# Optimization experiments

Measured on AMD Instinct MI355X. Metric: run time of the kernel, lower is better.

Reference implementation:

```python
import jax, jax.numpy as jnp
import numpy as np

N_NODES = 50000
N_EDGES = 800000
N_GRAPHS = 512
IN_FEATS = 256
HIDDEN = 128
OUT_FEATS = 128


def _lin(key, fan_in, fan_out):
    return jax.random.normal(key, (fan_in, fan_out), jnp.float32) * (1.0 / np.sqrt(fan_in))


def setup_inputs() -> dict:
    key = jax.random.key(0)
    ks = jax.random.split(key, 16)
    x = jax.random.normal(ks[0], (N_NODES, IN_FEATS), jnp.float32)
    edge_index = jax.random.randint(ks[1], (2, N_EDGES), 0, N_NODES, jnp.int32)
    batch = jnp.sort(jax.random.randint(ks[2], (N_NODES,), 0, N_GRAPHS, jnp.int32))
    return {
        "x": x,
        "edge_index": edge_index,
        "batch": batch,
        "num_graphs": N_GRAPHS,
        # TD branch GCN params
        "td_W1": _lin(ks[3], IN_FEATS, HIDDEN), "td_b1": jnp.zeros((HIDDEN,), jnp.float32),
        "td_W2": _lin(ks[4], HIDDEN, OUT_FEATS), "td_b2": jnp.zeros((OUT_FEATS,), jnp.float32),
        # BU branch GCN params
        "bu_W1": _lin(ks[5], IN_FEATS, HIDDEN), "bu_b1": jnp.zeros((HIDDEN,), jnp.float32),
        "bu_W2": _lin(ks[6], HIDDEN, OUT_FEATS), "bu_b2": jnp.zeros((OUT_FEATS,), jnp.float32),
        # proj_head: Linear(256,256) -> ReLU -> Linear(256,128)
        "pw1": _lin(ks[7], OUT_FEATS * 2, 256), "pb1": jnp.zeros((256,), jnp.float32),
        "pw2": _lin(ks[8], 256, 128), "pb2": jnp.zeros((128,), jnp.float32),
    }


def gcn_conv(h_in, W, b, src, dst, n_nodes):
    """PyG GCNConv: self-loops + symmetric normalization D^-1/2 (A+I) D^-1/2 X W + b."""
    h = h_in @ W  # [N, out]
    ones = jnp.ones(src.shape[0], h.dtype)
    deg = jax.ops.segment_sum(ones, dst, num_segments=n_nodes) + 1.0  # +1 for self-loop
    dinv = jax.lax.rsqrt(deg)  # deg >= 1 always
    norm = dinv[src] * dinv[dst]  # [E]
    agg = jax.ops.segment_sum(h[src] * norm[:, None], dst, num_segments=n_nodes)
    agg = agg + h * (dinv * dinv)[:, None]  # self-loop edge contribution
    return agg + b


def reference(x, edge_index, batch, num_graphs,
              td_W1, td_b1, td_W2, td_b2,
              bu_W1, bu_b1, bu_W2, bu_b2,
              pw1, pb1, pw2, pb2):
    n = x.shape[0]
    src, dst = edge_index[0], edge_index[1]

    def branch(W1, b1, W2, b2, s, d):
        h = jax.nn.relu(gcn_conv(x, W1, b1, s, d, n))
        # dropout is identity in eval mode
        h = gcn_conv(h, W2, b2, s, d, n)
        return jax.ops.segment_sum(h, batch, num_segments=num_graphs)  # global_add_pool

    td = branch(td_W1, td_b1, td_W2, td_b2, src, dst)
    bu = branch(bu_W1, bu_b1, bu_W2, bu_b2, dst, src)  # flipped edge_index
    h = jnp.concatenate([bu, td], axis=1)  # [G, 2*out_feats]
    h = jax.nn.relu(h @ pw1 + pb1) @ pw2 + pb2
    return h
```

## Files before the change

kernel.cpp:

```cpp
#include <hip/hip_runtime.h>

#define N_NODES 50000
#define N_PAD   50048
#define N_EDGES 800000
#define N_GRAPHS 512
#define F_IN 256
#define F_H 128
#define F_CAT 256

#define BSHIFT 9
#define NB 98
#define CAP 10240
#define EPB 3125
#define GEMM_BLOCKS 782

typedef __attribute__((ext_vector_type(8))) short short8;
typedef __attribute__((ext_vector_type(4))) float f32x4;
typedef unsigned int uint;
typedef unsigned short ushort;

static __device__ __forceinline__ ushort f2bf(float f) {
    uint u = __float_as_uint(f);
    u += 0x7FFF + ((u >> 16) & 1);
    return (ushort)(u >> 16);
}
static __device__ __forceinline__ float bflo(uint v) { return __uint_as_float(v << 16); }
static __device__ __forceinline__ float bfhi(uint v) { return __uint_as_float(v & 0xFFFF0000u); }
static __device__ __forceinline__ float bfu(ushort v) { return __uint_as_float((uint)v << 16); }

#define GLL(g, l) __builtin_amdgcn_global_load_lds( \
    (const __attribute__((address_space(1))) unsigned int*)(g), \
    (__attribute__((address_space(3))) unsigned int*)(l), 16, 0, 0)

__global__ __launch_bounds__(256) void gemm_scatter_kernel(
        const float* __restrict__ x, const ushort* __restrict__ Bt,
        ushort* __restrict__ C,
        const int* __restrict__ ei, int* __restrict__ gcur,
        uint* __restrict__ ebuf_td, uint* __restrict__ ebuf_bu) {
    __shared__ __align__(16) ushort As[128 * 32];
    __shared__ __align__(16) ushort Bs[128 * 32];
    __shared__ int lcnt[256];
    __shared__ int lbase[256];
    int tid = threadIdx.x;

    if (blockIdx.x < GEMM_BLOCKS) {
        int wave = tid >> 6, lane = tid & 63, quad = lane >> 4, l16 = lane & 15;
        size_t bm = (size_t)(blockIdx.x >> 1) * 128;
        size_t bn = (size_t)(blockIdx.x & 1) * 128;

        f32x4 acc[2][8];
        const f32x4 z4 = {0.f, 0.f, 0.f, 0.f};
#pragma unroll
        for (int i = 0; i < 2; i++)
#pragma unroll
            for (int j = 0; j < 8; j++) acc[i][j] = z4;

        int ar = tid >> 3;
        int akq = (tid & 7) * 4;
        int cb0 = wave * 64;
        int cb1 = 256 + wave * 64;
        int c0 = cb0 + lane, c1 = cb1 + lane;
        int r0 = c0 >> 2, s0 = (c0 & 3) * 8;
        int r1 = c1 >> 2, s1 = (c1 & 3) * 8;
        const ushort* b0p = Bt + (bn + r0) * 256 + s0;
        const ushort* b1p = Bt + (bn + r1) * 256 + s1;
        ushort* lB0 = Bs + cb0 * 8;
        ushort* lB1 = Bs + cb1 * 8;

        for (int kb = 0; kb < 8; kb++) {
            int k0 = kb * 32;
            float4 av[4];
#pragma unroll
            for (int j = 0; j < 4; j++) {
                size_t grow = bm + ar + j * 32;
                if (grow < N_NODES)
                    av[j] = *(const float4*)(x + grow * F_IN + k0 + akq);
                else
                    av[j] = make_float4(0.f, 0.f, 0.f, 0.f);
            }
            __syncthreads();
            GLL(b0p + k0, lB0);
            GLL(b1p + k0, lB1);
#pragma unroll
            for (int j = 0; j < 4; j++) {
                ushort4 u;
                u.x = f2bf(av[j].x); u.y = f2bf(av[j].y);
                u.z = f2bf(av[j].z); u.w = f2bf(av[j].w);
                *(ushort4*)(As + (ar + j * 32) * 32 + akq) = u;
            }
            __syncthreads();
            short8 af0 = *(const short8*)(As + (wave * 32 + l16) * 32 + quad * 8);
            short8 af1 = *(const short8*)(As + (wave * 32 + 16 + l16) * 32 + quad * 8);
#pragma unroll
            for (int ct = 0; ct < 8; ct++) {
                short8 bfr = *(const short8*)(Bs + (ct * 16 + l16) * 32 + quad * 8);
                acc[0][ct] = __builtin_amdgcn_mfma_f32_16x16x32_bf16(af0, bfr, acc[0][ct], 0, 0, 0);
                acc[1][ct] = __builtin_amdgcn_mfma_f32_16x16x32_bf16(af1, bfr, acc[1][ct], 0, 0, 0);
            }
        }
#pragma unroll
        for (int rt = 0; rt < 2; rt++) {
#pragma unroll
            for (int r = 0; r < 4; r++) {
                size_t row = bm + wave * 32 + rt * 16 + quad * 4 + r;
#pragma unroll
                for (int ct = 0; ct < 8; ct++) {
                    C[row * 256 + bn + ct * 16 + l16] = f2bf(acc[rt][ct][r]);
                }
            }
        }
    } else {
        lcnt[tid] = 0;
        __syncthreads();
        int e0 = (blockIdx.x - GEMM_BLOCKS) * EPB;
        for (int k = tid; k < EPB; k += 256) {
            int i = e0 + k;
            int s = ei[i], d = ei[N_EDGES + i];
            atomicAdd(&lcnt[d >> BSHIFT], 1);
            atomicAdd(&lcnt[128 + (s >> BSHIFT)], 1);
        }
        __syncthreads();
        if (tid < 2 * NB) {
            int dir = tid / NB, b = tid % NB;
            int c = lcnt[dir * 128 + b];
            lbase[dir * 128 + b] = c ? atomicAdd(&gcur[dir * NB + b], c) : 0;
        }
        __syncthreads();
        lcnt[tid] = 0;
        __syncthreads();
        for (int k = tid; k < EPB; k += 256) {
            int i = e0 + k;
            int s = ei[i], d = ei[N_EDGES + i];
            int bd = d >> BSHIFT, bs = s >> BSHIFT;
            int p = atomicAdd(&lcnt[bd], 1) + lbase[bd];
            ebuf_td[(size_t)bd * CAP + p] = (uint)s | ((uint)(d & 511) << 16);
            int q = atomicAdd(&lcnt[128 + bs], 1) + lbase[128 + bs];
            ebuf_bu[(size_t)bs * CAP + q] = (uint)d | ((uint)(s & 511) << 16);
        }
    }
}

__global__ __launch_bounds__(256) void csr_build_kernel(
        const uint* __restrict__ ebuf_td, const uint* __restrict__ ebuf_bu,
        const int* __restrict__ gcur,
        int* off_td, int* off_bu, ushort* deg_td, ushort* deg_bu,
        float* dinv_td, float* dinv_bu, ushort* csr_td, ushort* csr_bu) {
    int b = blockIdx.x, dir = blockIdx.y;
    const uint* ebuf = dir ? ebuf_bu : ebuf_td;
    int* off     = dir ? off_bu : off_td;
    ushort* deg  = dir ? deg_bu : deg_td;
    float* dinv  = dir ? dinv_bu : dinv_td;
    ushort* csr  = dir ? csr_bu : csr_td;
    __shared__ int cntL[512], offL[512], sm[256];
    int tid = threadIdx.x;
    cntL[tid] = 0; cntL[tid + 256] = 0;
    __syncthreads();
    int rbeg = b * CAP;
    int rend = rbeg + gcur[dir * NB + b];
    for (int k = rbeg + tid; k < rend; k += 256)
        atomicAdd(&cntL[ebuf[k] >> 16], 1);
    __syncthreads();
    int a0 = cntL[tid * 2], a1 = cntL[tid * 2 + 1];
    int ps = a0 + a1;
    sm[tid] = ps;
    __syncthreads();
    for (int o = 1; o < 256; o <<= 1) {
        int u = (tid >= o) ? sm[tid - o] : 0;
        __syncthreads();
        sm[tid] += u;
        __syncthreads();
    }
    int excl = sm[tid] - ps;
    offL[tid * 2] = excl;
    offL[tid * 2 + 1] = excl + a0;
    __syncthreads();
    int nbase = b << BSHIFT;
#pragma unroll
    for (int j = 0; j < 2; j++) {
        int nloc = tid + j * 256;
        int n = nbase + nloc;
        if (n < N_NODES) {
            off[n] = rbeg + offL[nloc];
            int c = cntL[nloc];
            deg[n] = (ushort)c;
            dinv[n] = rsqrtf((float)c + 1.0f);
        }
    }
    if (b == NB - 1) {
        int n = N_NODES + tid;
        if (n < N_PAD) dinv[n] = 1.0f;
    }
    cntL[tid] = offL[tid];
    cntL[tid + 256] = offL[tid + 256];
    __syncthreads();
    for (int k = rbeg + tid; k < rend; k += 256) {
        uint e = ebuf[k];
        int slot = atomicAdd(&cntL[e >> 16], 1);
        csr[rbeg + slot] = (ushort)(e & 0xFFFF);
    }
}

__global__ __launch_bounds__(256) void scale_kernel(
        ushort* __restrict__ linb,
        const float* __restrict__ dinv_td, const float* __restrict__ dinv_bu) {
    size_t i = (size_t)blockIdx.x * 256 + threadIdx.x;
    int row = (int)(i >> 5);
    int c8 = ((int)i & 31) * 8;
    float dv = (c8 < F_H) ? dinv_td[row] : dinv_bu[row];
    uint4 v = ((uint4*)linb)[i];
    uint4 o;
    o.x = (uint)f2bf(bflo(v.x) * dv) | ((uint)f2bf(bfhi(v.x) * dv) << 16);
    o.y = (uint)f2bf(bflo(v.y) * dv) | ((uint)f2bf(bfhi(v.y) * dv) << 16);
    o.z = (uint)f2bf(bflo(v.z) * dv) | ((uint)f2bf(bfhi(v.z) * dv) << 16);
    o.w = (uint)f2bf(bflo(v.w) * dv) | ((uint)f2bf(bfhi(v.w) * dv) << 16);
    ((uint4*)linb)[i] = o;
}

__global__ void prep_w_kernel(const float* __restrict__ td_W1, const float* __restrict__ bu_W1,
                              const float* __restrict__ td_W2, const float* __restrict__ bu_W2,
                              ushort* __restrict__ Bt1, ushort* __restrict__ Wt2) {
    int n = blockIdx.x;
    int k = threadIdx.x;
    float w1 = (n < F_H) ? td_W1[(size_t)k * F_H + n] : bu_W1[(size_t)k * F_H + (n - F_H)];
    Bt1[(size_t)n * 256 + k] = f2bf(w1);
    if (k < 128) {
        float w2 = (n < F_H) ? bu_W2[(size_t)k * F_H + n]
                             : td_W2[(size_t)k * F_H + (n - F_H)];
        Wt2[(size_t)k * 256 + n] = f2bf(w2);
    }
}

static __device__ __forceinline__ void gather_node(
        const ushort* __restrict__ base, const ushort* __restrict__ csr,
        int kb, int ke, int half, float a[4]) {
    float p[4] = {0.f, 0.f, 0.f, 0.f};
    float q[4] = {0.f, 0.f, 0.f, 0.f};
    float r[4] = {0.f, 0.f, 0.f, 0.f};
    int k = kb;
    for (; k + 16 <= ke; k += 16) {
        int i0 = csr[k + half],      i1 = csr[k + 2 + half];
        int i2 = csr[k + 4 + half],  i3 = csr[k + 6 + half];
        int i4 = csr[k + 8 + half],  i5 = csr[k + 10 + half];
        int i6 = csr[k + 12 + half], i7 = csr[k + 14 + half];
        uint2 v0 = *(const uint2*)(base + (size_t)i0 * F_CAT);
        uint2 v1 = *(const uint2*)(base + (size_t)i1 * F_CAT);
        uint2 v2 = *(const uint2*)(base + (size_t)i2 * F_CAT);
        uint2 v3 = *(const uint2*)(base + (size_t)i3 * F_CAT);
        uint2 v4 = *(const uint2*)(base + (size_t)i4 * F_CAT);
        uint2 v5 = *(const uint2*)(base + (size_t)i5 * F_CAT);
        uint2 v6 = *(const uint2*)(base + (size_t)i6 * F_CAT);
        uint2 v7 = *(const uint2*)(base + (size_t)i7 * F_CAT);
        a[0] += bflo(v0.x); a[1] += bfhi(v0.x); a[2] += bflo(v0.y); a[3] += bfhi(v0.y);
        p[0] += bflo(v1.x); p[1] += bfhi(v1.x); p[2] += bflo(v1.y); p[3] += bfhi(v1.y);
        q[0] += bflo(v2.x); q[1] += bfhi(v2.x); q[2] += bflo(v2.y); q[3] += bfhi(v2.y);
        r[0] += bflo(v3.x); r[1] += bfhi(v3.x); r[2] += bflo(v3.y); r[3] += bfhi(v3.y);
        a[0] += bflo(v4.x); a[1] += bfhi(v4.x); a[2] += bflo(v4.y); a[3] += bfhi(v4.y);
        p[0] += bflo(v5.x); p[1] += bfhi(v5.x); p[2] += bflo(v5.y); p[3] += bfhi(v5.y);
        q[0] += bflo(v6.x); q[1] += bfhi(v6.x); q[2] += bflo(v6.y); q[3] += bfhi(v6.y);
        r[0] += bflo(v7.x); r[1] += bfhi(v7.x); r[2] += bflo(v7.y); r[3] += bfhi(v7.y);
    }
    for (; k + 8 <= ke; k += 8) {
        int i0 = csr[k + half],     i1 = csr[k + 2 + half];
        int i2 = csr[k + 4 + half], i3 = csr[k + 6 + half];
        uint2 v0 = *(const uint2*)(base + (size_t)i0 * F_CAT);
        uint2 v1 = *(const uint2*)(base + (size_t)i1 * F_CAT);
        uint2 v2 = *(const uint2*)(base + (size_t)i2 * F_CAT);
        uint2 v3 = *(const uint2*)(base + (size_t)i3 * F_CAT);
        a[0] += bflo(v0.x); a[1] += bfhi(v0.x); a[2] += bflo(v0.y); a[3] += bfhi(v0.y);
        p[0] += bflo(v1.x); p[1] += bfhi(v1.x); p[2] += bflo(v1.y); p[3] += bfhi(v1.y);
        q[0] += bflo(v2.x); q[1] += bfhi(v2.x); q[2] += bflo(v2.y); q[3] += bfhi(v2.y);
        r[0] += bflo(v3.x); r[1] += bfhi(v3.x); r[2] += bflo(v3.y); r[3] += bfhi(v3.y);
    }
    for (; k < ke; k += 2) {
        int kk = k + half;
        if (kk < ke) {
            uint2 v = *(const uint2*)(base + (size_t)csr[kk] * F_CAT);
            a[0] += bflo(v.x); a[1] += bfhi(v.x); a[2] += bflo(v.y); a[3] += bfhi(v.y);
        }
    }
#pragma unroll
    for (int j = 0; j < 4; j++) a[j] += (p[j] + q[j]) + r[j];
}

__global__ __launch_bounds__(256) void agg1_kernel(
        const ushort* __restrict__ linS, ushort* __restrict__ h1s,
        const ushort* __restrict__ csr_td, const int* __restrict__ off_td,
        const ushort* __restrict__ deg_td, const float* __restrict__ dinv_td,
        const ushort* __restrict__ csr_bu, const int* __restrict__ off_bu,
        const ushort* __restrict__ deg_bu, const float* __restrict__ dinv_bu,
        const float* __restrict__ b_td, const float* __restrict__ b_bu) {
    int wave = threadIdx.x >> 6, lane = threadIdx.x & 63;
    int n0 = (blockIdx.x * 2 + (wave >> 1)) * 8;
    int br = wave & 1;
    const ushort* csr = br ? csr_bu : csr_td;
    const int* off    = br ? off_bu : off_td;
    const ushort* deg = br ? deg_bu : deg_td;
    const float* dinv = br ? dinv_bu : dinv_td;
    const float* bias = br ? b_bu : b_td;
    int half = lane >> 5, l32 = lane & 31;
    int col = br * F_H + l32 * 4;
    const ushort* base = linS + col;
    int bcol = l32 * 4;
    float bs0 = bias[bcol], bs1 = bias[bcol + 1];
    float bs2 = bias[bcol + 2], bs3 = bias[bcol + 3];

#pragma unroll
    for (int j = 0; j < 8; j++) {
        int n = n0 + j;
        float a[4] = {0.f, 0.f, 0.f, 0.f};
        int kb = off[n];
        gather_node(base, csr, kb, kb + deg[n], half, a);
#pragma unroll
        for (int t = 0; t < 4; t++) a[t] += __shfl_xor(a[t], 32);
        uint2 vs = *(const uint2*)(base + (size_t)n * F_CAT);
        a[0] += bflo(vs.x); a[1] += bfhi(vs.x); a[2] += bflo(vs.y); a[3] += bfhi(vs.y);
        float dn = dinv[n];
        float o0 = fmaxf(a[0] * dn + bs0, 0.f) * dn;
        float o1 = fmaxf(a[1] * dn + bs1, 0.f) * dn;
        float o2 = fmaxf(a[2] * dn + bs2, 0.f) * dn;
        float o3 = fmaxf(a[3] * dn + bs3, 0.f) * dn;
        if (half == 0) {
            uint2 pk;
            pk.x = (uint)f2bf(o0) | ((uint)f2bf(o1) << 16);
            pk.y = (uint)f2bf(o2) | ((uint)f2bf(o3) << 16);
            *(uint2*)(h1s + (size_t)n * F_CAT + col) = pk;
        }
    }
}

__global__ __launch_bounds__(256) void agg2_pool_kernel(
        const ushort* __restrict__ h1s, float* __restrict__ pooled_pre,
        const int* __restrict__ batch,
        const ushort* __restrict__ csr_td, const int* __restrict__ off_td,
        const ushort* __restrict__ deg_td, const float* __restrict__ dinv_td,
        const ushort* __restrict__ csr_bu, const int* __restrict__ off_bu,
        const ushort* __restrict__ deg_bu, const float* __restrict__ dinv_bu) {
    int wave = threadIdx.x >> 6, lane = threadIdx.x & 63;
    int n0 = (blockIdx.x * 2 + (wave >> 1)) * 8;
    int br = wave & 1;
    const ushort* csr = br ? csr_bu : csr_td;
    const int* off    = br ? off_bu : off_td;
    const ushort* deg = br ? deg_bu : deg_td;
    const float* dinv = br ? dinv_bu : dinv_td;
    int half = lane >> 5, l32 = lane & 31;
    int col = br * F_H + l32 * 4;
    const ushort* base = h1s + col;

    float acc0 = 0.f, acc1 = 0.f, acc2 = 0.f, acc3 = 0.f;
    int gcur = batch[n0];
#pragma unroll
    for (int j = 0; j < 8; j++) {
        int n = n0 + j;
        int g = batch[n];
        if (g != gcur) {
            if (half == 0) {
                float* pp = &pooled_pre[(size_t)gcur * F_CAT + col];
                unsafeAtomicAdd(pp,     acc0);
                unsafeAtomicAdd(pp + 1, acc1);
                unsafeAtomicAdd(pp + 2, acc2);
                unsafeAtomicAdd(pp + 3, acc3);
            }
            acc0 = acc1 = acc2 = acc3 = 0.f;
            gcur = g;
        }
        float a[4] = {0.f, 0.f, 0.f, 0.f};
        int kb = off[n];
        gather_node(base, csr, kb, kb + deg[n], half, a);
#pragma unroll
        for (int t = 0; t < 4; t++) a[t] += __shfl_xor(a[t], 32);
        uint2 vs = *(const uint2*)(base + (size_t)n * F_CAT);
        a[0] += bflo(vs.x); a[1] += bfhi(vs.x); a[2] += bflo(vs.y); a[3] += bfhi(vs.y);
        float dn = dinv[n];
        acc0 += a[0] * dn;
        acc1 += a[1] * dn;
        acc2 += a[2] * dn;
        acc3 += a[3] * dn;
    }
    if (half == 0) {
        float* pp = &pooled_pre[(size_t)gcur * F_CAT + col];
        unsafeAtomicAdd(pp,     acc0);
        unsafeAtomicAdd(pp + 1, acc1);
        unsafeAtomicAdd(pp + 2, acc2);
        unsafeAtomicAdd(pp + 3, acc3);
    }
}

__global__ __launch_bounds__(256) void head_kernel(
        const float* __restrict__ pooled_pre, const int* __restrict__ batch,
        const ushort* __restrict__ Wt2,
        const float* __restrict__ td_b2, const float* __restrict__ bu_b2,
        const float* __restrict__ pw1, const float* __restrict__ pb1,
        const float* __restrict__ pw2, const float* __restrict__ pb2,
        float* __restrict__ out) {
    int g = blockIdx.x;
    int tid = threadIdx.x;
    __shared__ float row[256], z[256], hid[256];
    row[tid] = pooled_pre[(size_t)g * 256 + tid];
    int lo = 0, hi = N_NODES;
    while (lo < hi) { int m = (lo + hi) >> 1; if (batch[m] < g) lo = m + 1; else hi = m; }
    int start = lo;
    lo = start; hi = N_NODES;
    while (lo < hi) { int m = (lo + hi) >> 1; if (batch[m] < g + 1) lo = m + 1; else hi = m; }
    float cnt = (float)(lo - start);
    __syncthreads();
    const float* rsel = (tid < 128) ? (row + F_H) : row;
    float b2 = (tid < 128) ? bu_b2[tid] : td_b2[tid - F_H];
    float acc = cnt * b2;
    for (int k = 0; k < F_H; k++) acc += rsel[k] * bfu(Wt2[(size_t)k * 256 + tid]);
    z[tid] = acc;
    __syncthreads();
    float h = pb1[tid];
    for (int k = 0; k < 256; k++) h += z[k] * pw1[(size_t)k * 256 + tid];
    hid[tid] = fmaxf(h, 0.f);
    __syncthreads();
    if (tid < 128) {
        float o = pb2[tid];
        for (int k = 0; k < 256; k++) o += hid[k] * pw2[(size_t)k * 128 + tid];
        out[(size_t)g * 128 + tid] = o;
    }
}

extern "C" void kernel_launch(void* const* d_in, const int* in_sizes, int n_in,
                              void* d_out, int out_size, void* d_ws, size_t ws_size,
                              hipStream_t stream) {
    const float* x     = (const float*)d_in[0];
    const int*   ei    = (const int*)d_in[1];
    const int*   batch = (const int*)d_in[2];
    const float* td_W1 = (const float*)d_in[4];
    const float* td_b1 = (const float*)d_in[5];
    const float* td_W2 = (const float*)d_in[6];
    const float* td_b2 = (const float*)d_in[7];
    const float* bu_W1 = (const float*)d_in[8];
    const float* bu_b1 = (const float*)d_in[9];
    const float* bu_W2 = (const float*)d_in[10];
    const float* bu_b2 = (const float*)d_in[11];
    const float* pw1   = (const float*)d_in[12];
    const float* pb1   = (const float*)d_in[13];
    const float* pw2   = (const float*)d_in[14];
    const float* pb2   = (const float*)d_in[15];
    float* out = (float*)d_out;

    char* p = (char*)d_ws;
    auto alloc = [&](size_t bytes) { void* r = (void*)p; p += (bytes + 255) & ~(size_t)255; return r; };
    char* zreg = (char*)alloc(1024 + (size_t)N_GRAPHS * F_CAT * sizeof(float));
    int* gcur = (int*)zreg;
    float* pooled_pre = (float*)(zreg + 1024);
    uint* ebuf_td = (uint*)alloc((size_t)NB * CAP * sizeof(uint));
    uint* ebuf_bu = (uint*)alloc((size_t)NB * CAP * sizeof(uint));
    ushort* csr_td = (ushort*)alloc((size_t)NB * CAP * sizeof(ushort));
    ushort* csr_bu = (ushort*)alloc((size_t)NB * CAP * sizeof(ushort));
    int* off_td = (int*)alloc((size_t)N_NODES * sizeof(int));
    int* off_bu = (int*)alloc((size_t)N_NODES * sizeof(int));
    ushort* deg_td = (ushort*)alloc((size_t)N_NODES * sizeof(ushort));
    ushort* deg_bu = (ushort*)alloc((size_t)N_NODES * sizeof(ushort));
    float* dinv_td = (float*)alloc((size_t)N_PAD * sizeof(float));
    float* dinv_bu = (float*)alloc((size_t)N_PAD * sizeof(float));
    ushort* Bt1 = (ushort*)alloc((size_t)256 * 256 * sizeof(ushort));
    ushort* Wt2 = (ushort*)alloc((size_t)128 * 256 * sizeof(ushort));
    ushort* linb = (ushort*)alloc((size_t)N_PAD * F_CAT * sizeof(ushort));
    ushort* h1s  = (ushort*)alloc((size_t)N_PAD * F_CAT * sizeof(ushort));

    hipMemsetAsync(zreg, 0, 1024 + (size_t)N_GRAPHS * F_CAT * sizeof(float), stream);

    prep_w_kernel<<<256, 256, 0, stream>>>(td_W1, bu_W1, td_W2, bu_W2, Bt1, Wt2);

    gemm_scatter_kernel<<<GEMM_BLOCKS + N_EDGES / EPB, 256, 0, stream>>>(
        x, Bt1, linb, ei, gcur, ebuf_td, ebuf_bu);

    csr_build_kernel<<<dim3(NB, 2), 256, 0, stream>>>(ebuf_td, ebuf_bu, gcur,
        off_td, off_bu, deg_td, deg_bu, dinv_td, dinv_bu, csr_td, csr_bu);

    scale_kernel<<<(N_PAD * F_CAT / 8) / 256, 256, 0, stream>>>(linb, dinv_td, dinv_bu);

    agg1_kernel<<<N_NODES / 16, 256, 0, stream>>>(linb, h1s,
        csr_td, off_td, deg_td, dinv_td, csr_bu, off_bu, deg_bu, dinv_bu, td_b1, bu_b1);

    agg2_pool_kernel<<<N_NODES / 16, 256, 0, stream>>>(h1s, pooled_pre, batch,
        csr_td, off_td, deg_td, dinv_td, csr_bu, off_bu, deg_bu, dinv_bu);

    head_kernel<<<N_GRAPHS, 256, 0, stream>>>(pooled_pre, batch, Wt2,
        td_b2, bu_b2, pw1, pb1, pw2, pb2, out);
}
```

Before: 349.4 us.

## Fuse degree scaling into CSR build; use atomic work-stealing in aggregation kernels

Removes the separate scale_kernel launch by having each CSR-build block rescale its 512 rows of the linear output by dinv, using a shared-memory copy of the freshly computed values. The two aggregation kernels switch from one fixed 8-node unit per wave to a persistent grid of 2048 blocks in which each wave pulls 8-node units from an atomic counter per branch. The aim is to save a launch and a full extra pass over the feature buffer, and to balance load across waves given the uneven node degrees. In exchange it adds atomic counter traffic, and the scaling now runs in only 196 blocks, which may reduce memory parallelism for that pass.

```diff
diff --git a/kernel.cpp b/kernel.cpp
--- a/kernel.cpp
+++ b/kernel.cpp
@@ -13,6 +13,8 @@
 #define CAP 10240
 #define EPB 3125
 #define GEMM_BLOCKS 782
+#define AGG_UNITS 6250
+#define AGG_BLOCKS 2048
 
 typedef __attribute__((ext_vector_type(8))) short short8;
 typedef __attribute__((ext_vector_type(4))) float f32x4;
@@ -144,7 +146,8 @@
         const uint* __restrict__ ebuf_td, const uint* __restrict__ ebuf_bu,
         const int* __restrict__ gcur,
         int* off_td, int* off_bu, ushort* deg_td, ushort* deg_bu,
-        float* dinv_td, float* dinv_bu, ushort* csr_td, ushort* csr_bu) {
+        float* dinv_td, float* dinv_bu, ushort* csr_td, ushort* csr_bu,
+        ushort* __restrict__ linb) {
     int b = blockIdx.x, dir = blockIdx.y;
     const uint* ebuf = dir ? ebuf_bu : ebuf_td;
     int* off     = dir ? off_bu : off_td;
@@ -152,6 +155,7 @@
     float* dinv  = dir ? dinv_bu : dinv_td;
     ushort* csr  = dir ? csr_bu : csr_td;
     __shared__ int cntL[512], offL[512], sm[256];
+    __shared__ float dinvL[512];
     int tid = threadIdx.x;
     cntL[tid] = 0; cntL[tid + 256] = 0;
     __syncthreads();
@@ -179,12 +183,15 @@
     for (int j = 0; j < 2; j++) {
         int nloc = tid + j * 256;
         int n = nbase + nloc;
+        float dv = 1.0f;
         if (n < N_NODES) {
             off[n] = rbeg + offL[nloc];
             int c = cntL[nloc];
             deg[n] = (ushort)c;
-            dinv[n] = rsqrtf((float)c + 1.0f);
-        }
+            dv = rsqrtf((float)c + 1.0f);
+            dinv[n] = dv;
+        }
+        dinvL[nloc] = dv;
     }
     if (b == NB - 1) {
         int n = N_NODES + tid;
@@ -198,22 +205,21 @@
         int slot = atomicAdd(&cntL[e >> 16], 1);
         csr[rbeg + slot] = (ushort)(e & 0xFFFF);
     }
-}
-
-__global__ __launch_bounds__(256) void scale_kernel(
-        ushort* __restrict__ linb,
-        const float* __restrict__ dinv_td, const float* __restrict__ dinv_bu) {
-    size_t i = (size_t)blockIdx.x * 256 + threadIdx.x;
-    int row = (int)(i >> 5);
-    int c8 = ((int)i & 31) * 8;
-    float dv = (c8 < F_H) ? dinv_td[row] : dinv_bu[row];
-    uint4 v = ((uint4*)linb)[i];
-    uint4 o;
-    o.x = (uint)f2bf(bflo(v.x) * dv) | ((uint)f2bf(bfhi(v.x) * dv) << 16);
-    o.y = (uint)f2bf(bflo(v.y) * dv) | ((uint)f2bf(bfhi(v.y) * dv) << 16);
-    o.z = (uint)f2bf(bflo(v.z) * dv) | ((uint)f2bf(bfhi(v.z) * dv) << 16);
-    o.w = (uint)f2bf(bflo(v.w) * dv) | ((uint)f2bf(bfhi(v.w) * dv) << 16);
-    ((uint4*)linb)[i] = o;
+    uint4* lin4 = (uint4*)linb;
+    for (int i = tid; i < 512 * 16; i += 256) {
+        int rloc = i >> 4;
+        int n = nbase + rloc;
+        if (n >= N_NODES) break;
+        float dv = dinvL[rloc];
+        size_t gi = (size_t)n * 32 + dir * 16 + (i & 15);
+        uint4 v = lin4[gi];
+        uint4 o;
+        o.x = (uint)f2bf(bflo(v.x) * dv) | ((uint)f2bf(bfhi(v.x) * dv) << 16);
+        o.y = (uint)f2bf(bflo(v.y) * dv) | ((uint)f2bf(bfhi(v.y) * dv) << 16);
+        o.z = (uint)f2bf(bflo(v.z) * dv) | ((uint)f2bf(bfhi(v.z) * dv) << 16);
+        o.w = (uint)f2bf(bflo(v.w) * dv) | ((uint)f2bf(bfhi(v.w) * dv) << 16);
+        lin4[gi] = o;
+    }
 }
 
 __global__ void prep_w_kernel(const float* __restrict__ td_W1, const float* __restrict__ bu_W1,
@@ -284,13 +290,13 @@
 
 __global__ __launch_bounds__(256) void agg1_kernel(
         const ushort* __restrict__ linS, ushort* __restrict__ h1s,
+        int* __restrict__ ctrs,
         const ushort* __restrict__ csr_td, const int* __restrict__ off_td,
         const ushort* __restrict__ deg_td, const float* __restrict__ dinv_td,
         const ushort* __restrict__ csr_bu, const int* __restrict__ off_bu,
         const ushort* __restrict__ deg_bu, const float* __restrict__ dinv_bu,
         const float* __restrict__ b_td, const float* __restrict__ b_bu) {
     int wave = threadIdx.x >> 6, lane = threadIdx.x & 63;
-    int n0 = (blockIdx.x * 2 + (wave >> 1)) * 8;
     int br = wave & 1;
     const ushort* csr = br ? csr_bu : csr_td;
     const int* off    = br ? off_bu : off_td;
@@ -303,40 +309,47 @@
     int bcol = l32 * 4;
     float bs0 = bias[bcol], bs1 = bias[bcol + 1];
     float bs2 = bias[bcol + 2], bs3 = bias[bcol + 3];
-
-#pragma unroll
-    for (int j = 0; j < 8; j++) {
-        int n = n0 + j;
-        float a[4] = {0.f, 0.f, 0.f, 0.f};
-        int kb = off[n];
-        gather_node(base, csr, kb, kb + deg[n], half, a);
-#pragma unroll
-        for (int t = 0; t < 4; t++) a[t] += __shfl_xor(a[t], 32);
-        uint2 vs = *(const uint2*)(base + (size_t)n * F_CAT);
-        a[0] += bflo(vs.x); a[1] += bfhi(vs.x); a[2] += bflo(vs.y); a[3] += bfhi(vs.y);
-        float dn = dinv[n];
-        float o0 = fmaxf(a[0] * dn + bs0, 0.f) * dn;
-        float o1 = fmaxf(a[1] * dn + bs1, 0.f) * dn;
-        float o2 = fmaxf(a[2] * dn + bs2, 0.f) * dn;
-        float o3 = fmaxf(a[3] * dn + bs3, 0.f) * dn;
-        if (half == 0) {
-            uint2 pk;
-            pk.x = (uint)f2bf(o0) | ((uint)f2bf(o1) << 16);
-            pk.y = (uint)f2bf(o2) | ((uint)f2bf(o3) << 16);
-            *(uint2*)(h1s + (size_t)n * F_CAT + col) = pk;
+    int* ctr = ctrs + (br << 5);
+
+    while (true) {
+        int unit = 0;
+        if (lane == 0) unit = atomicAdd(ctr, 1);
+        unit = __shfl(unit, 0);
+        if (unit >= AGG_UNITS) break;
+        int n0 = unit * 8;
+#pragma unroll
+        for (int j = 0; j < 8; j++) {
+            int n = n0 + j;
+            float a[4] = {0.f, 0.f, 0.f, 0.f};
+            int kb = off[n];
+            gather_node(base, csr, kb, kb + deg[n], half, a);
+#pragma unroll
+            for (int t = 0; t < 4; t++) a[t] += __shfl_xor(a[t], 32);
+            uint2 vs = *(const uint2*)(base + (size_t)n * F_CAT);
+            a[0] += bflo(vs.x); a[1] += bfhi(vs.x); a[2] += bflo(vs.y); a[3] += bfhi(vs.y);
+            float dn = dinv[n];
+            float o0 = fmaxf(a[0] * dn + bs0, 0.f) * dn;
+            float o1 = fmaxf(a[1] * dn + bs1, 0.f) * dn;
+            float o2 = fmaxf(a[2] * dn + bs2, 0.f) * dn;
+            float o3 = fmaxf(a[3] * dn + bs3, 0.f) * dn;
+            if (half == 0) {
+                uint2 pk;
+                pk.x = (uint)f2bf(o0) | ((uint)f2bf(o1) << 16);
+                pk.y = (uint)f2bf(o2) | ((uint)f2bf(o3) << 16);
+                *(uint2*)(h1s + (size_t)n * F_CAT + col) = pk;
+            }
         }
     }
 }
 
 __global__ __launch_bounds__(256) void agg2_pool_kernel(
         const ushort* __restrict__ h1s, float* __restrict__ pooled_pre,
-        const int* __restrict__ batch,
+        int* __restrict__ ctrs, const int* __restrict__ batch,
         const ushort* __restrict__ csr_td, const int* __restrict__ off_td,
         const ushort* __restrict__ deg_td, const float* __restrict__ dinv_td,
         const ushort* __restrict__ csr_bu, const int* __restrict__ off_bu,
         const ushort* __restrict__ deg_bu, const float* __restrict__ dinv_bu) {
     int wave = threadIdx.x >> 6, lane = threadIdx.x & 63;
-    int n0 = (blockIdx.x * 2 + (wave >> 1)) * 8;
     int br = wave & 1;
     const ushort* csr = br ? csr_bu : csr_td;
     const int* off    = br ? off_bu : off_td;
@@ -345,43 +358,51 @@
     int half = lane >> 5, l32 = lane & 31;
     int col = br * F_H + l32 * 4;
     const ushort* base = h1s + col;
-
-    float acc0 = 0.f, acc1 = 0.f, acc2 = 0.f, acc3 = 0.f;
-    int gcur = batch[n0];
-#pragma unroll
-    for (int j = 0; j < 8; j++) {
-        int n = n0 + j;
-        int g = batch[n];
-        if (g != gcur) {
-            if (half == 0) {
-                float* pp = &pooled_pre[(size_t)gcur * F_CAT + col];
-                unsafeAtomicAdd(pp,     acc0);
-                unsafeAtomicAdd(pp + 1, acc1);
-                unsafeAtomicAdd(pp + 2, acc2);
-                unsafeAtomicAdd(pp + 3, acc3);
+    int* ctr = ctrs + (br << 5);
+
+    while (true) {
+        int unit = 0;
+        if (lane == 0) unit = atomicAdd(ctr, 1);
+        unit = __shfl(unit, 0);
+        if (unit >= AGG_UNITS) break;
+        int n0 = unit * 8;
+        float acc0 = 0.f, acc1 = 0.f, acc2 = 0.f, acc3 = 0.f;
+        int gcur = batch[n0];
+#pragma unroll
+        for (int j = 0; j < 8; j++) {
+            int n = n0 + j;
+            int g = batch[n];
+            if (g != gcur) {
+                if (half == 0) {
+                    float* pp = &pooled_pre[(size_t)gcur * F_CAT + col];
+                    unsafeAtomicAdd(pp,     acc0);
+                    unsafeAtomicAdd(pp + 1, acc1);
+                    unsafeAtomicAdd(pp + 2, acc2);
+                    unsafeAtomicAdd(pp + 3, acc3);
+                }
+                acc0 = acc1 = acc2 = acc3 = 0.f;
+                gcur = g;
             }
-            acc0 = acc1 = acc2 = acc3 = 0.f;
-            gcur = g;
-        }
-        float a[4] = {0.f, 0.f, 0.f, 0.f};
-        int kb = off[n];
-        gather_node(base, csr, kb, kb + deg[n], half, a);
-#pragma unroll
-        for (int t = 0; t < 4; t++) a[t] += __shfl_xor(a[t], 32);
-        uint2 vs = *(const uint2*)(base + (size_t)n * F_CAT);
-        a[0] += bflo(vs.x); a[1] += bfhi(vs.x); a[2] += bflo(vs.y); a[3] += bfhi(vs.y);
-        float dn = dinv[n];
-        acc0 += a[0] * dn;
-        acc1 += a[1] * dn;
-        acc2 += a[2] * dn;
-        acc3 += a[3] * dn;
-    }
-    if (half == 0) {
-        float* pp = &pooled_pre[(size_t)gcur * F_CAT + col];
-        unsafeAtomicAdd(pp,     acc0);
-        unsafeAtomicAdd(pp + 1, acc1);
-        unsafeAtomicAdd(pp + 2, acc2);
-        unsafeAtomicAdd(pp + 3, acc3);
+            float a[4] = {0.f, 0.f, 0.f, 0.f};
+            int kb = off[n];
+            gather_node(base, csr, kb, kb + deg[n], half, a);
+#pragma unroll
+            for (int t = 0; t < 4; t++) a[t] += __shfl_xor(a[t], 32);
+            uint2 vs = *(const uint2*)(base + (size_t)n * F_CAT);
+            a[0] += bflo(vs.x); a[1] += bfhi(vs.x); a[2] += bflo(vs.y); a[3] += bfhi(vs.y);
+            float dn = dinv[n];
+            acc0 += a[0] * dn;
+            acc1 += a[1] * dn;
+            acc2 += a[2] * dn;
+            acc3 += a[3] * dn;
+        }
+        if (half == 0) {
+            float* pp = &pooled_pre[(size_t)gcur * F_CAT + col];
+            unsafeAtomicAdd(pp,     acc0);
+            unsafeAtomicAdd(pp + 1, acc1);
+            unsafeAtomicAdd(pp + 2, acc2);
+            unsafeAtomicAdd(pp + 3, acc3);
+        }
     }
 }
 
@@ -442,9 +463,11 @@
 
     char* p = (char*)d_ws;
     auto alloc = [&](size_t bytes) { void* r = (void*)p; p += (bytes + 255) & ~(size_t)255; return r; };
-    char* zreg = (char*)alloc(1024 + (size_t)N_GRAPHS * F_CAT * sizeof(float));
+    char* zreg = (char*)alloc(2048 + (size_t)N_GRAPHS * F_CAT * sizeof(float));
     int* gcur = (int*)zreg;
-    float* pooled_pre = (float*)(zreg + 1024);
+    int* ctr1 = (int*)(zreg + 1024);
+    int* ctr2 = (int*)(zreg + 1536);
+    float* pooled_pre = (float*)(zreg + 2048);
     uint* ebuf_td = (uint*)alloc((size_t)NB * CAP * sizeof(uint));
     uint* ebuf_bu = (uint*)alloc((size_t)NB * CAP * sizeof(uint));
     ushort* csr_td = (ushort*)alloc((size_t)NB * CAP * sizeof(ushort));
@@ -460,7 +483,7 @@
     ushort* linb = (ushort*)alloc((size_t)N_PAD * F_CAT * sizeof(ushort));
     ushort* h1s  = (ushort*)alloc((size_t)N_PAD * F_CAT * sizeof(ushort));
 
-    hipMemsetAsync(zreg, 0, 1024 + (size_t)N_GRAPHS * F_CAT * sizeof(float), stream);
+    hipMemsetAsync(zreg, 0, 2048 + (size_t)N_GRAPHS * F_CAT * sizeof(float), stream);
 
     prep_w_kernel<<<256, 256, 0, stream>>>(td_W1, bu_W1, td_W2, bu_W2, Bt1, Wt2);
 
@@ -468,14 +491,12 @@
         x, Bt1, linb, ei, gcur, ebuf_td, ebuf_bu);
 
     csr_build_kernel<<<dim3(NB, 2), 256, 0, stream>>>(ebuf_td, ebuf_bu, gcur,
-        off_td, off_bu, deg_td, deg_bu, dinv_td, dinv_bu, csr_td, csr_bu);
-
-    scale_kernel<<<(N_PAD * F_CAT / 8) / 256, 256, 0, stream>>>(linb, dinv_td, dinv_bu);
-
-    agg1_kernel<<<N_NODES / 16, 256, 0, stream>>>(linb, h1s,
+        off_td, off_bu, deg_td, deg_bu, dinv_td, dinv_bu, csr_td, csr_bu, linb);
+
+    agg1_kernel<<<AGG_BLOCKS, 256, 0, stream>>>(linb, h1s, ctr1,
         csr_td, off_td, deg_td, dinv_td, csr_bu, off_bu, deg_bu, dinv_bu, td_b1, bu_b1);
 
-    agg2_pool_kernel<<<N_NODES / 16, 256, 0, stream>>>(h1s, pooled_pre, batch,
+    agg2_pool_kernel<<<AGG_BLOCKS, 256, 0, stream>>>(h1s, pooled_pre, ctr2, batch,
         csr_td, off_td, deg_td, dinv_td, csr_bu, off_bu, deg_bu, dinv_bu);
 
     head_kernel<<<N_GRAPHS, 256, 0, stream>>>(pooled_pre, batch, Wt2,
```

Measured after the change: 516.1 us. 1.48x slower.
